# Kernel tuning notes

Measured on AMD Instinct MI355X. Metric: run time of the kernel, lower is better.

## Reference

```python
import jax, jax.numpy as jnp
import numpy as np

N_NODES = 40000            # num nodes (maybe_num_nodes)
E = 2_560_000              # input edges
SENTINEL = N_NODES * N_NODES  # key for masked-out edges; sorts last; fits int32 (1.6e9 < 2^31)


def setup_inputs() -> dict:
    key = jax.random.key(0)
    k1, k2 = jax.random.split(key)
    edge_index = jax.random.randint(k1, (2, E), 0, N_NODES, dtype=jnp.int32)
    edge_attr = jax.random.uniform(k2, (E,), dtype=jnp.float32)
    t = jnp.full((1,), 0.5, dtype=jnp.float32)  # learnable threshold parameter
    return {"edge_index": edge_index, "edge_attr": edge_attr, "t": t}


def reference(edge_index, edge_attr, t):
    """Threshold mask -> symmetrize -> coalesce (sort by (row,col), sum duplicates).

    JAX has static shapes, so compaction is expressed as masking: dropped edges get
    key=SENTINEL (sorts last) and attr contribution 0. Returns padded outputs of
    fixed size 2E plus the count of valid (unique, kept) edges. Invalid slots have
    edge_index == -1 and edge_attr == 0.
    """
    row, col = edge_index[0], edge_index[1]
    mask = edge_attr <= t[0]                      # [E] bool
    # symmetrize: stack (row,col) and (col,row), duplicate attrs  -> [2E]
    r2 = jnp.concatenate([row, col])
    c2 = jnp.concatenate([col, row])
    a2 = jnp.concatenate([edge_attr, edge_attr])
    m2 = jnp.concatenate([mask, mask])
    # coalesce: linearize key = row*N + col, sort, segment-sum duplicates
    key = jnp.where(m2, r2 * N_NODES + c2, SENTINEL)   # [2E] int32
    order = jnp.argsort(key)
    key_s = key[order]
    a_s = jnp.where(m2, a2, 0.0)[order]
    E2 = key_s.shape[0]
    new_seg = jnp.concatenate([jnp.ones((1,), bool), key_s[1:] != key_s[:-1]])
    seg = jnp.cumsum(new_seg.astype(jnp.int32)) - 1    # segment id per sorted edge
    vals = jax.ops.segment_sum(a_s, seg, num_segments=E2, indices_are_sorted=True)
    uk = jnp.full((E2,), SENTINEL, dtype=key_s.dtype).at[seg].set(key_s)
    valid = uk < SENTINEL
    out_row = jnp.where(valid, uk // N_NODES, -1)
    out_col = jnp.where(valid, uk % N_NODES, -1)
    edge_index_out = jnp.stack([out_row, out_col])     # [2, 2E] padded with -1
    edge_attr_out = jnp.where(valid, vals, 0.0)        # [2E]   padded with 0
    num_edges = jnp.sum(valid.astype(jnp.int32))
    return edge_index_out, edge_attr_out, num_edges
```

## Files before the change

kernel.cpp:

```cpp
#include <hip/hip_runtime.h>
#include <stdint.h>

#define NN 40000
#define E_IN 2560000
#define E2 5120000
#define NFINE 2500
#define NSB 20
#define SB_SHIFT 11
#define FINES_PER_SB 128
#define P2_TILES 66
#define SBCAP (P2_TILES*2048)
#define CAPB 1280

typedef unsigned long long ull;

__global__ void k_init(int* __restrict__ sbCursor, int* __restrict__ fineCursor) {
    int tid = threadIdx.x;
    for (int f = tid; f < NFINE; f += 256) fineCursor[f] = f * CAPB;
    if (tid < NSB) sbCursor[tid] = tid * SBCAP;
}

__global__ void __launch_bounds__(256) k_part1(const int* __restrict__ ei,
                                               const float* __restrict__ ea,
                                               const float* __restrict__ t,
                                               int* __restrict__ sbCursor,
                                               ull* __restrict__ pairs1) {
    __shared__ ull staged[2048];
    __shared__ int cnt[NSB], off[NSB + 1], gbase[NSB];
    int tid = threadIdx.x;
    if (tid < NSB) cnt[tid] = 0;
    __syncthreads();
    float t0 = t[0];
    int tileStart = blockIdx.x * 1024;

    ull eA[4], eB[4];
    int rkA[4], rkB[4];
    bool keep[4];
#pragma unroll
    for (int k = 0; k < 4; k++) {
        int i = tileStart + tid + k * 256;
        float a = ea[i];
        keep[k] = (a <= t0);
        if (keep[k]) {
            int r = ei[i], c = ei[E_IN + i];
            unsigned ab = __float_as_uint(a);
            eA[k] = ((ull)(unsigned)r << 48) | ((ull)(unsigned)c << 32) | ab;
            eB[k] = ((ull)(unsigned)c << 48) | ((ull)(unsigned)r << 32) | ab;
            rkA[k] = atomicAdd(&cnt[r >> SB_SHIFT], 1);
            rkB[k] = atomicAdd(&cnt[c >> SB_SHIFT], 1);
        }
    }
    __syncthreads();
    if (tid == 0) {
        int acc = 0;
        for (int s = 0; s < NSB; s++) { off[s] = acc; acc += cnt[s]; }
        off[NSB] = acc;
    }
    __syncthreads();
    if (tid < NSB) gbase[tid] = atomicAdd(&sbCursor[tid], cnt[tid]);
#pragma unroll
    for (int k = 0; k < 4; k++) {
        if (keep[k]) {
            staged[off[(int)(eA[k] >> 59)] + rkA[k]] = eA[k];
            staged[off[(int)(eB[k] >> 59)] + rkB[k]] = eB[k];
        }
    }
    __syncthreads();
    int total = off[NSB];
    for (int i = tid; i < total; i += 256) {
        ull e = staged[i];
        int sb = (int)(e >> 59);
        pairs1[gbase[sb] + (i - off[sb])] = e;
    }
}

__global__ void __launch_bounds__(256) k_part2(const int* __restrict__ sbCursor,
                                               int* __restrict__ fineCursor,
                                               const ull* __restrict__ pairs1,
                                               ull* __restrict__ pairs2) {
    int sb = blockIdx.x / P2_TILES;
    int tile = blockIdx.x % P2_TILES;
    int regionBase = sb * SBCAP;
    int len = sbCursor[sb] - regionBase;
    if (len > SBCAP) len = SBCAP;
    int start = tile * 2048;
    if (start >= len) return;
    int cntT = len - start; if (cntT > 2048) cntT = 2048;
    const ull* src = pairs1 + regionBase + start;

    int fineFirst = sb * FINES_PER_SB;
    int nF = NFINE - fineFirst; if (nF > FINES_PER_SB) nF = FINES_PER_SB;

    __shared__ ull staged[2048];
    __shared__ int cnt[FINES_PER_SB], off[FINES_PER_SB + 1], gbase[FINES_PER_SB];
    int tid = threadIdx.x;
    if (tid < FINES_PER_SB) { cnt[tid] = 0; gbase[tid] = 0; }
    __syncthreads();

    ull e[8];
    int rk[8];
#pragma unroll
    for (int k = 0; k < 8; k++) {
        int i = tid + k * 256;
        if (i < cntT) {
            e[k] = src[i];
            rk[k] = atomicAdd(&cnt[(int)(e[k] >> 52) & 127], 1);
        }
    }
    __syncthreads();
    if (tid == 0) {
        int acc = 0;
        for (int s = 0; s < FINES_PER_SB; s++) { off[s] = acc; acc += cnt[s]; }
        off[FINES_PER_SB] = acc;
    }
    __syncthreads();
    if (tid < nF) gbase[tid] = atomicAdd(&fineCursor[fineFirst + tid], cnt[tid]);
#pragma unroll
    for (int k = 0; k < 8; k++) {
        int i = tid + k * 256;
        if (i < cntT) staged[off[(int)(e[k] >> 52) & 127] + rk[k]] = e[k];
    }
    __syncthreads();
    int total = off[FINES_PER_SB];
    for (int i = tid; i < total; i += 256) {
        ull v = staged[i];
        int lb = (int)(v >> 52) & 127;
        pairs2[gbase[lb] + (i - off[lb])] = v;
    }
}

__device__ __forceinline__ void ce(ull& a, ull& b) {
    ull mn = a < b ? a : b;
    ull mx = a < b ? b : a;
    a = mn; b = mx;
}
__device__ __forceinline__ void sort8(ull* v) {
    ce(v[0],v[1]); ce(v[2],v[3]); ce(v[4],v[5]); ce(v[6],v[7]);
    ce(v[0],v[2]); ce(v[1],v[3]); ce(v[4],v[6]); ce(v[5],v[7]);
    ce(v[1],v[2]); ce(v[5],v[6]);
    ce(v[0],v[4]); ce(v[1],v[5]); ce(v[2],v[6]); ce(v[3],v[7]);
    ce(v[2],v[4]); ce(v[3],v[5]);
    ce(v[1],v[2]); ce(v[3],v[4]); ce(v[5],v[6]);
}
__device__ __forceinline__ void sort16(ull* v) {
    sort8(v); sort8(v + 8);
    ce(v[0],v[8]);  ce(v[1],v[9]);  ce(v[2],v[10]); ce(v[3],v[11]);
    ce(v[4],v[12]); ce(v[5],v[13]); ce(v[6],v[14]); ce(v[7],v[15]);
    ce(v[4],v[8]);  ce(v[5],v[9]);  ce(v[6],v[10]); ce(v[7],v[11]);
    ce(v[2],v[4]);  ce(v[3],v[5]);  ce(v[6],v[8]);  ce(v[7],v[9]);  ce(v[10],v[12]); ce(v[11],v[13]);
    ce(v[1],v[2]);  ce(v[3],v[4]);  ce(v[5],v[6]);  ce(v[7],v[8]);  ce(v[9],v[10]);  ce(v[11],v[12]); ce(v[13],v[14]);
}

__global__ void __launch_bounds__(512) k_sortrows(const int* __restrict__ fineCursor,
                                                  ull* __restrict__ pairs2,
                                                  int* __restrict__ uniqueCount) {
    int b = blockIdx.x;
    int base = b * CAPB;
    int n = fineCursor[b] - base;
    if (n > CAPB) n = CAPB;
    __shared__ ull d[CAPB];
    __shared__ int cnt[512], off[512], wsum[8], ucnt[16], ubase[16];
    int tid = threadIdx.x;
    int lane = tid & 63;
    cnt[tid] = 0;
    __syncthreads();

    ull e[3]; int rk[3], sbk[3];
#pragma unroll
    for (int k = 0; k < 3; k++) {
        int i = tid + k * 512;
        if (i < n) {
            e[k] = pairs2[base + i];
            sbk[k] = (int)(e[k] >> 43) & 511;
            rk[k] = atomicAdd(&cnt[sbk[k]], 1);
        }
    }
    __syncthreads();

    int x = cnt[tid];
    int incl = x;
#pragma unroll
    for (int dlt = 1; dlt < 64; dlt <<= 1) {
        int y = __shfl_up(incl, dlt, 64);
        if (lane >= dlt) incl += y;
    }
    if (lane == 63) wsum[tid >> 6] = incl;
    __syncthreads();
    if (tid == 0) {
        int a = 0;
        for (int w = 0; w < 8; w++) { int tt = wsum[w]; wsum[w] = a; a += tt; }
    }
    __syncthreads();
    off[tid] = wsum[tid >> 6] + incl - x;
    __syncthreads();

#pragma unroll
    for (int k = 0; k < 3; k++) {
        int i = tid + k * 512;
        if (i < n) d[off[sbk[k]] + rk[k]] = e[k];
    }
    __syncthreads();

    int cn = cnt[tid]; if (cn > 16) cn = 16;
    int o0 = off[tid];
    ull v[16];
    bool big = __any(cn > 8);
    if (!big) {
#pragma unroll
        for (int k = 0; k < 8; k++) v[k] = (k < cn) ? d[o0 + k] : ~0ull;
        sort8(v);
    } else {
#pragma unroll
        for (int k = 0; k < 16; k++) v[k] = (k < cn) ? d[o0 + k] : ~0ull;
        sort16(v);
    }

    int uc = (cn > 0) ? 1 : 0;
#pragma unroll
    for (int k = 1; k < 16; k++)
        if (k < cn && (unsigned)(v[k] >> 32) != (unsigned)(v[k - 1] >> 32)) uc++;

    int uincl = uc;
#pragma unroll
    for (int dlt = 1; dlt < 64; dlt <<= 1) {
        int y = __shfl_up(uincl, dlt, 64);
        if (lane >= dlt) uincl += y;
    }
    int rowTot0 = __shfl(uincl, 31, 64);
    int rr = tid >> 5;
    int rowOff = uincl - uc - ((lane >= 32) ? rowTot0 : 0);
    if (lane == 31) ucnt[rr] = uincl;
    if (lane == 63) ucnt[rr] = uincl - rowTot0;
    __syncthreads();
    if (tid == 0) {
        int acc = 0;
        for (int s = 0; s < 16; s++) { ubase[s] = acc; acc += ucnt[s]; }
        uniqueCount[b] = acc;
    }
    __syncthreads();

    if (cn > 0) {
        ull* dst = pairs2 + base + ubase[rr] + rowOff;
        unsigned curKey = (unsigned)(v[0] >> 32);
        float curSum = __uint_as_float((unsigned)v[0]);
        int em = 0;
#pragma unroll
        for (int k = 1; k < 16; k++) {
            if (k < cn) {
                unsigned key = (unsigned)(v[k] >> 32);
                float a = __uint_as_float((unsigned)v[k]);
                if (key == curKey) {
                    curSum += a;
                } else {
                    dst[em] = ((ull)curKey << 32) | __float_as_uint(curSum);
                    em++;
                    curKey = key; curSum = a;
                }
            }
        }
        dst[em] = ((ull)curKey << 32) | __float_as_uint(curSum);
    }
}

__global__ void __launch_bounds__(1024) k_scan(const int* __restrict__ in, int n,
                                               int* __restrict__ outExcl,
                                               float* __restrict__ totalDst) {
    __shared__ int partial[1024];
    int tid = threadIdx.x;
    int start = tid * 3;
    int v[3], sum = 0;
#pragma unroll
    for (int k = 0; k < 3; k++) {
        int i = start + k;
        int x = (i < n) ? in[i] : 0;
        v[k] = sum;
        sum += x;
    }
    partial[tid] = sum;
    __syncthreads();
    for (int off = 1; off < 1024; off <<= 1) {
        int add = (tid >= off) ? partial[tid - off] : 0;
        __syncthreads();
        partial[tid] += add;
        __syncthreads();
    }
    int base = partial[tid] - sum;
#pragma unroll
    for (int k = 0; k < 3; k++) {
        int i = start + k;
        if (i < n) outExcl[i] = base + v[k];
    }
    if (tid == 1023) {
        outExcl[n] = partial[1023];
        if (totalDst) totalDst[0] = (float)partial[1023];
    }
}

__global__ void __launch_bounds__(256) k_outfill(const int* __restrict__ outBase,
                                                 const ull* __restrict__ pairs2,
                                                 float* __restrict__ out) {
    __shared__ int sOB[NFINE + 1];
    int tid = threadIdx.x;
    for (int i = tid; i <= NFINE; i += 256) sOB[i] = outBase[i];
    __syncthreads();
    int j0 = (blockIdx.x * 256 + tid) * 4;
    int T = sOB[NFINE];
    float rr[4], cc[4], aa[4];
    int lo = 0;
    if (j0 < T) {
        int hi = NFINE;
        while (hi - lo > 1) {
            int mid = (lo + hi) >> 1;
            if (sOB[mid] <= j0) lo = mid; else hi = mid;
        }
    }
#pragma unroll
    for (int k = 0; k < 4; k++) {
        int j = j0 + k;
        if (j < T) {
            while (lo < NFINE - 1 && sOB[lo + 1] <= j) lo++;
            ull e = pairs2[lo * CAPB + (j - sOB[lo])];
            rr[k] = (float)(int)(e >> 48);
            cc[k] = (float)(int)((e >> 32) & 0xFFFF);
            aa[k] = __uint_as_float((unsigned)(e & 0xFFFFFFFFu));
        } else { rr[k] = -1.0f; cc[k] = -1.0f; aa[k] = 0.0f; }
    }
    *(float4*)(out + j0)          = make_float4(rr[0], rr[1], rr[2], rr[3]);
    *(float4*)(out + E2 + j0)     = make_float4(cc[0], cc[1], cc[2], cc[3]);
    *(float4*)(out + 2 * E2 + j0) = make_float4(aa[0], aa[1], aa[2], aa[3]);
}

extern "C" void kernel_launch(void* const* d_in, const int* in_sizes, int n_in,
                              void* d_out, int out_size, void* d_ws, size_t ws_size,
                              hipStream_t stream) {
    const int*   ei = (const int*)d_in[0];
    const float* ea = (const float*)d_in[1];
    const float* t  = (const float*)d_in[2];
    float* out = (float*)d_out;

    int* sbCursor    = (int*)d_ws;
    int* fineCursor  = sbCursor + 32;
    int* uniqueCount = fineCursor + NFINE;
    int* outBase     = uniqueCount + NFINE;
    ull* pairs2 = (ull*)(((uintptr_t)(outBase + NFINE + 1) + 15) & ~(uintptr_t)15);

    ull* pairs1 = (ull*)d_out;

    k_init<<<1, 256, 0, stream>>>(sbCursor, fineCursor);
    k_part1<<<E_IN / 1024, 256, 0, stream>>>(ei, ea, t, sbCursor, pairs1);
    k_part2<<<NSB * P2_TILES, 256, 0, stream>>>(sbCursor, fineCursor, pairs1, pairs2);
    k_sortrows<<<NFINE, 512, 0, stream>>>(fineCursor, pairs2, uniqueCount);
    k_scan<<<1, 1024, 0, stream>>>(uniqueCount, NFINE, outBase, out + (size_t)3 * E2);
    k_outfill<<<E2 / 1024, 256, 0, stream>>>(outBase, pairs2, out);
}
```

Baseline: 175.9 us.

## Pad global cursors, privatize per-wave bin counters, vectorize loads, use shuffle scans

Spaces the global sbCursor and fineCursor atomics 16 ints apart so each counter sits on its own cache line instead of sharing one. In k_part1, edges are loaded as float4/int4 per thread, and shared-memory bin counters are split per wave to cut atomic contention. The serial single-thread bin prefix is replaced by a wave shuffle scan, and k_scan's log-step shared-memory scan with many barriers becomes a two-level wave shuffle scan. Loading 4 contiguous edges per thread changes which thread handles which edge, so the order within each bin differs, but the later sort makes the output unaffected.

```diff
diff --git a/kernel.cpp b/kernel.cpp
--- a/kernel.cpp
+++ b/kernel.cpp
@@ -11,13 +11,14 @@
 #define P2_TILES 66
 #define SBCAP (P2_TILES*2048)
 #define CAPB 1280
+#define CSTR 16
 
 typedef unsigned long long ull;
 
 __global__ void k_init(int* __restrict__ sbCursor, int* __restrict__ fineCursor) {
     int tid = threadIdx.x;
-    for (int f = tid; f < NFINE; f += 256) fineCursor[f] = f * CAPB;
-    if (tid < NSB) sbCursor[tid] = tid * SBCAP;
+    for (int f = tid; f < NFINE; f += 256) fineCursor[f * CSTR] = f * CAPB;
+    if (tid < NSB) sbCursor[tid * CSTR] = tid * SBCAP;
 }
 
 __global__ void __launch_bounds__(256) k_part1(const int* __restrict__ ei,
@@ -26,43 +27,62 @@
                                                int* __restrict__ sbCursor,
                                                ull* __restrict__ pairs1) {
     __shared__ ull staged[2048];
-    __shared__ int cnt[NSB], off[NSB + 1], gbase[NSB];
-    int tid = threadIdx.x;
-    if (tid < NSB) cnt[tid] = 0;
+    __shared__ int cntW[NSB * 4];
+    __shared__ int off[NSB + 1], wb[NSB * 4], gbase[NSB];
+    int tid = threadIdx.x;
+    int wave = tid >> 6;
+    if (tid < NSB * 4) cntW[tid] = 0;
     __syncthreads();
     float t0 = t[0];
-    int tileStart = blockIdx.x * 1024;
+    int i0 = blockIdx.x * 1024 + tid * 4;
+
+    float4 a4 = *(const float4*)(ea + i0);
+    int4 r4 = *(const int4*)(ei + i0);
+    int4 c4 = *(const int4*)(ei + E_IN + i0);
+    float av[4] = {a4.x, a4.y, a4.z, a4.w};
+    int rv[4] = {r4.x, r4.y, r4.z, r4.w};
+    int cv[4] = {c4.x, c4.y, c4.z, c4.w};
 
     ull eA[4], eB[4];
     int rkA[4], rkB[4];
     bool keep[4];
 #pragma unroll
     for (int k = 0; k < 4; k++) {
-        int i = tileStart + tid + k * 256;
-        float a = ea[i];
-        keep[k] = (a <= t0);
+        keep[k] = (av[k] <= t0);
         if (keep[k]) {
-            int r = ei[i], c = ei[E_IN + i];
-            unsigned ab = __float_as_uint(a);
-            eA[k] = ((ull)(unsigned)r << 48) | ((ull)(unsigned)c << 32) | ab;
-            eB[k] = ((ull)(unsigned)c << 48) | ((ull)(unsigned)r << 32) | ab;
-            rkA[k] = atomicAdd(&cnt[r >> SB_SHIFT], 1);
-            rkB[k] = atomicAdd(&cnt[c >> SB_SHIFT], 1);
-        }
-    }
-    __syncthreads();
-    if (tid == 0) {
-        int acc = 0;
-        for (int s = 0; s < NSB; s++) { off[s] = acc; acc += cnt[s]; }
-        off[NSB] = acc;
-    }
-    __syncthreads();
-    if (tid < NSB) gbase[tid] = atomicAdd(&sbCursor[tid], cnt[tid]);
+            unsigned ab = __float_as_uint(av[k]);
+            eA[k] = ((ull)(unsigned)rv[k] << 48) | ((ull)(unsigned)cv[k] << 32) | ab;
+            eB[k] = ((ull)(unsigned)cv[k] << 48) | ((ull)(unsigned)rv[k] << 32) | ab;
+            rkA[k] = atomicAdd(&cntW[((rv[k] >> SB_SHIFT) << 2) | wave], 1);
+            rkB[k] = atomicAdd(&cntW[((cv[k] >> SB_SHIFT) << 2) | wave], 1);
+        }
+    }
+    __syncthreads();
+    if (tid < NSB) {
+        int s = tid;
+        int c0 = cntW[s * 4], c1 = cntW[s * 4 + 1], c2 = cntW[s * 4 + 2], c3 = cntW[s * 4 + 3];
+        int tot = c0 + c1 + c2 + c3;
+        int incl = tot;
+#pragma unroll
+        for (int d = 1; d < 32; d <<= 1) {
+            int y = __shfl_up(incl, d, 64);
+            if (s >= d) incl += y;
+        }
+        int o = incl - tot;
+        off[s] = o;
+        if (s == NSB - 1) off[NSB] = incl;
+        wb[s * 4]     = o;
+        wb[s * 4 + 1] = o + c0;
+        wb[s * 4 + 2] = o + c0 + c1;
+        wb[s * 4 + 3] = o + c0 + c1 + c2;
+        gbase[s] = atomicAdd(&sbCursor[s * CSTR], tot);
+    }
+    __syncthreads();
 #pragma unroll
     for (int k = 0; k < 4; k++) {
         if (keep[k]) {
-            staged[off[(int)(eA[k] >> 59)] + rkA[k]] = eA[k];
-            staged[off[(int)(eB[k] >> 59)] + rkB[k]] = eB[k];
+            staged[wb[(((int)(eA[k] >> 59)) << 2) | wave] + rkA[k]] = eA[k];
+            staged[wb[(((int)(eB[k] >> 59)) << 2) | wave] + rkB[k]] = eB[k];
         }
     }
     __syncthreads();
@@ -81,7 +101,7 @@
     int sb = blockIdx.x / P2_TILES;
     int tile = blockIdx.x % P2_TILES;
     int regionBase = sb * SBCAP;
-    int len = sbCursor[sb] - regionBase;
+    int len = sbCursor[sb * CSTR] - regionBase;
     if (len > SBCAP) len = SBCAP;
     int start = tile * 2048;
     if (start >= len) return;
@@ -114,7 +134,7 @@
         off[FINES_PER_SB] = acc;
     }
     __syncthreads();
-    if (tid < nF) gbase[tid] = atomicAdd(&fineCursor[fineFirst + tid], cnt[tid]);
+    if (tid < nF) gbase[tid] = atomicAdd(&fineCursor[(fineFirst + tid) * CSTR], cnt[tid]);
 #pragma unroll
     for (int k = 0; k < 8; k++) {
         int i = tid + k * 256;
@@ -156,7 +176,7 @@
                                                   int* __restrict__ uniqueCount) {
     int b = blockIdx.x;
     int base = b * CAPB;
-    int n = fineCursor[b] - base;
+    int n = fineCursor[b * CSTR] - base;
     if (n > CAPB) n = CAPB;
     __shared__ ull d[CAPB];
     __shared__ int cnt[512], off[512], wsum[8], ucnt[16], ubase[16];
@@ -265,8 +285,8 @@
 __global__ void __launch_bounds__(1024) k_scan(const int* __restrict__ in, int n,
                                                int* __restrict__ outExcl,
                                                float* __restrict__ totalDst) {
-    __shared__ int partial[1024];
-    int tid = threadIdx.x;
+    __shared__ int wsum[16];
+    int tid = threadIdx.x, lane = tid & 63, w = tid >> 6;
     int start = tid * 3;
     int v[3], sum = 0;
 #pragma unroll
@@ -276,23 +296,35 @@
         v[k] = sum;
         sum += x;
     }
-    partial[tid] = sum;
-    __syncthreads();
-    for (int off = 1; off < 1024; off <<= 1) {
-        int add = (tid >= off) ? partial[tid - off] : 0;
-        __syncthreads();
-        partial[tid] += add;
-        __syncthreads();
-    }
-    int base = partial[tid] - sum;
+    int incl = sum;
+#pragma unroll
+    for (int d = 1; d < 64; d <<= 1) {
+        int y = __shfl_up(incl, d, 64);
+        if (lane >= d) incl += y;
+    }
+    if (lane == 63) wsum[w] = incl;
+    __syncthreads();
+    if (tid < 16) {
+        int x2 = wsum[tid];
+        int incl2 = x2;
+#pragma unroll
+        for (int d = 1; d < 16; d <<= 1) {
+            int y = __shfl_up(incl2, d, 64);
+            if (tid >= d) incl2 += y;
+        }
+        wsum[tid] = incl2 - x2;
+    }
+    __syncthreads();
+    int base = wsum[w] + incl - sum;
 #pragma unroll
     for (int k = 0; k < 3; k++) {
         int i = start + k;
         if (i < n) outExcl[i] = base + v[k];
     }
     if (tid == 1023) {
-        outExcl[n] = partial[1023];
-        if (totalDst) totalDst[0] = (float)partial[1023];
+        int tot = base + sum;
+        outExcl[n] = tot;
+        if (totalDst) totalDst[0] = (float)tot;
     }
 }
 
@@ -339,8 +371,8 @@
     float* out = (float*)d_out;
 
     int* sbCursor    = (int*)d_ws;
-    int* fineCursor  = sbCursor + 32;
-    int* uniqueCount = fineCursor + NFINE;
+    int* fineCursor  = sbCursor + NSB * CSTR;
+    int* uniqueCount = fineCursor + NFINE * CSTR;
     int* outBase     = uniqueCount + NFINE;
     ull* pairs2 = (ull*)(((uintptr_t)(outBase + NFINE + 1) + 15) & ~(uintptr_t)15);
 
```

After: 197.2 us. 12.1% more time.
